# Kernel optimization log

Measured on AMD Instinct MI355X. Metric: run time of the kernel, lower is better.

Reference implementation:

```python
import jax, jax.numpy as jnp
import numpy as np


def setup_inputs() -> dict:
    key = jax.random.key(0)
    ks = jax.random.split(key, 6)
    B, Q, K = 4, 512, 1024
    Dq, Dk, Dv, H = 512, 512, 512, 128
    return {
        "queries": jax.random.normal(ks[0], (B, Q, Dq), dtype=jnp.float32),
        "keys": jax.random.normal(ks[1], (B, K, Dk), dtype=jnp.float32),
        "values": jax.random.normal(ks[2], (B, K, Dv), dtype=jnp.float32),
        "W_q": jax.random.normal(ks[3], (Dq, H), dtype=jnp.float32) / np.sqrt(Dq),
        "W_k": jax.random.normal(ks[4], (Dk, H), dtype=jnp.float32) / np.sqrt(Dk),
        "w_v": jax.random.normal(ks[5], (H,), dtype=jnp.float32) / np.sqrt(H),
    }


def reference(queries, keys, values, W_q, W_k, w_v):
    # Additive (Bahdanau) attention.
    q = jnp.einsum("bqd,dh->bqh", queries, W_q)          # [B,Q,H]
    k = jnp.einsum("bkd,dh->bkh", keys, W_k)             # [B,K,H]
    features = jnp.tanh(q[:, :, None, :] + k[:, None, :, :])  # [B,Q,K,H]
    scores = jnp.einsum("bqkh,h->bqk", features, w_v)    # [B,Q,K]
    attn = jax.nn.softmax(scores, axis=-1)               # [B,Q,K]
    return jnp.einsum("bqk,bkv->bqv", attn, values)      # [B,Q,Dv]
```

## Files before the change

### kernel.cpp

```cpp
#include <hip/hip_runtime.h>

#define BB   4
#define QS   512
#define KSZ  1024
#define DD   512
#define HH   128
#define DVV  512

typedef unsigned int uint;
typedef unsigned short ushort;
typedef __attribute__((ext_vector_type(8)))  short short8;
typedef __attribute__((ext_vector_type(16))) float f32x16;

__device__ __forceinline__ float rcp_fast(float x)  { return __builtin_amdgcn_rcpf(x); }
__device__ __forceinline__ float exp2_fast(float x) { return __builtin_amdgcn_exp2f(x); }

__device__ __forceinline__ void split1(float v, short& h, short& l) {
    uint u = __float_as_uint(v);
    h = (short)(u >> 16);
    float r = v - __uint_as_float(u & 0xffff0000u);
    l = (short)(__float_as_uint(r) >> 16);
}

__global__ __launch_bounds__(256) void proj_exp_kernel(
    const float* __restrict__ q,  const float* __restrict__ k,
    const float* __restrict__ Wq, const float* __restrict__ Wk,
    float* __restrict__ eq, float* __restrict__ ek, int nq_blocks)
{
    __shared__ float At[16][36];
    __shared__ float Wt[32][128];

    const float* A; const float* W; float* outp; int m0;
    if ((int)blockIdx.x < nq_blocks) {
        A = q;  W = Wq; outp = eq; m0 = blockIdx.x * 16;
    } else {
        A = k;  W = Wk; outp = ek; m0 = (blockIdx.x - nq_blocks) * 16;
    }

    const int tid = threadIdx.x;
    const int h4  = tid & 31;
    const int r   = tid >> 5;

    float4 acc0 = {0.f,0.f,0.f,0.f};
    float4 acc1 = {0.f,0.f,0.f,0.f};

    for (int d0 = 0; d0 < DD; d0 += 32) {
        if (tid < 128) {
            int row = tid >> 3, c4 = tid & 7;
            *(float4*)&At[row][c4 * 4] =
                *(const float4*)&A[(size_t)(m0 + row) * DD + d0 + c4 * 4];
        }
        #pragma unroll
        for (int i = 0; i < 4; i++) {
            int f = tid + i * 256;
            int row = f >> 5, c4 = f & 31;
            *(float4*)&Wt[row][c4 * 4] =
                *(const float4*)&W[(size_t)(d0 + row) * HH + c4 * 4];
        }
        __syncthreads();
        #pragma unroll 4
        for (int kk = 0; kk < 32; kk++) {
            float4 w4 = *(const float4*)&Wt[kk][h4 * 4];
            float a0 = At[r][kk];
            float a1 = At[r + 8][kk];
            acc0.x = fmaf(a0, w4.x, acc0.x); acc0.y = fmaf(a0, w4.y, acc0.y);
            acc0.z = fmaf(a0, w4.z, acc0.z); acc0.w = fmaf(a0, w4.w, acc0.w);
            acc1.x = fmaf(a1, w4.x, acc1.x); acc1.y = fmaf(a1, w4.y, acc1.y);
            acc1.z = fmaf(a1, w4.z, acc1.z); acc1.w = fmaf(a1, w4.w, acc1.w);
        }
        __syncthreads();
    }

    const float C2L = 2.8853900817779268f;
    float4 o0, o1;
    o0.x = exp2_fast(acc0.x * C2L); o0.y = exp2_fast(acc0.y * C2L);
    o0.z = exp2_fast(acc0.z * C2L); o0.w = exp2_fast(acc0.w * C2L);
    o1.x = exp2_fast(acc1.x * C2L); o1.y = exp2_fast(acc1.y * C2L);
    o1.z = exp2_fast(acc1.z * C2L); o1.w = exp2_fast(acc1.w * C2L);
    *(float4*)&outp[(size_t)(m0 + r)     * HH + h4 * 4] = o0;
    *(float4*)&outp[(size_t)(m0 + r + 8) * HH + h4 * 4] = o1;
}

__global__ __launch_bounds__(256) void vt_kernel(
    const float* __restrict__ val, ushort* __restrict__ vhi, ushort* __restrict__ vlo)
{
    __shared__ float Ts[32][33];
    const int b  = blockIdx.z;
    const int k0 = blockIdx.x * 32;
    const int n0 = blockIdx.y * 32;
    const int tid = threadIdx.x;

    {
        const int kk = tid >> 3, n4 = (tid & 7) * 4;
        float4 v = *(const float4*)&val[((size_t)b * KSZ + k0 + kk) * DVV + n0 + n4];
        Ts[kk][n4 + 0] = v.x; Ts[kk][n4 + 1] = v.y;
        Ts[kk][n4 + 2] = v.z; Ts[kk][n4 + 3] = v.w;
    }
    __syncthreads();
    {
        const int nn = tid >> 3, k4 = (tid & 7) * 4;
        ushort h[4], l[4];
        #pragma unroll
        for (int i = 0; i < 4; i++) {
            short hh, ll;
            split1(Ts[k4 + i][nn], hh, ll);
            h[i] = (ushort)hh; l[i] = (ushort)ll;
        }
        size_t o = ((size_t)b * DVV + n0 + nn) * KSZ + k0 + k4;
        *(ushort4*)&vhi[o] = make_ushort4(h[0], h[1], h[2], h[3]);
        *(ushort4*)&vlo[o] = make_ushort4(l[0], l[1], l[2], l[3]);
    }
}

__global__ __launch_bounds__(256) void scores_kernel(
    const float* __restrict__ eq, const float* __restrict__ ek,
    const float* __restrict__ wv, float* __restrict__ P, float* __restrict__ rsp)
{
    __shared__ float eqs[64][68];
    __shared__ float eks[64][68];
    __shared__ float wvs[HH];

    const int tid = threadIdx.x;
    const int b  = blockIdx.z;
    const int q0 = blockIdx.y * 64;
    const int k0 = blockIdx.x * 64;

    const float* eqb = eq + ((size_t)b * QS  + q0) * HH;
    const float* ekb = ek + ((size_t)b * KSZ + k0) * HH;

    if (tid < 32) *(float4*)&wvs[tid * 4] = *(const float4*)&wv[tid * 4];

    const int tk = tid & 15;
    const int tq = tid >> 4;

    float acc[4][4] = {};

    for (int hc = 0; hc < HH; hc += 64) {
        __syncthreads();
        #pragma unroll
        for (int i = 0; i < 4; i++) {
            int f = tid + i * 256;
            int row = f >> 4, c4 = f & 15;
            *(float4*)&eqs[row][c4 * 4] =
                *(const float4*)&eqb[(size_t)row * HH + hc + c4 * 4];
            *(float4*)&eks[row][c4 * 4] =
                *(const float4*)&ekb[(size_t)row * HH + hc + c4 * 4];
        }
        __syncthreads();

        for (int h0 = 0; h0 < 64; h0 += 4) {
            float4 wv4 = *(const float4*)&wvs[hc + h0];
            float4 eq4[4], ek4[4];
            #pragma unroll
            for (int j = 0; j < 4; j++) {
                eq4[j] = *(const float4*)&eqs[tq + 16 * j][h0];
                ek4[j] = *(const float4*)&eks[tk + 16 * j][h0];
            }
            #pragma unroll
            for (int jq = 0; jq < 4; jq++) {
                #pragma unroll
                for (int jk = 0; jk < 4; jk++) {
                    acc[jq][jk] = fmaf(wv4.x, rcp_fast(fmaf(eq4[jq].x, ek4[jk].x, 1.0f)), acc[jq][jk]);
                    acc[jq][jk] = fmaf(wv4.y, rcp_fast(fmaf(eq4[jq].y, ek4[jk].y, 1.0f)), acc[jq][jk]);
                    acc[jq][jk] = fmaf(wv4.z, rcp_fast(fmaf(eq4[jq].z, ek4[jk].z, 1.0f)), acc[jq][jk]);
                    acc[jq][jk] = fmaf(wv4.w, rcp_fast(fmaf(eq4[jq].w, ek4[jk].w, 1.0f)), acc[jq][jk]);
                }
            }
        }
    }

    const float CN = -2.8853900817779268f;
    float* pb = P + ((size_t)b * QS + q0) * KSZ + k0;
    #pragma unroll
    for (int jq = 0; jq < 4; jq++) {
        float rowp = 0.f;
        #pragma unroll
        for (int jk = 0; jk < 4; jk++) {
            float pv_ = exp2_fast(acc[jq][jk] * CN);
            pb[(size_t)(tq + 16 * jq) * KSZ + tk + 16 * jk] = pv_;
            rowp += pv_;
        }
        #pragma unroll
        for (int m = 8; m; m >>= 1) rowp += __shfl_xor(rowp, m);
        if ((tid & 15) == 0)
            rsp[((size_t)b * QS + q0 + tq + 16 * jq) * 16 + blockIdx.x] = rowp;
    }
}

__global__ __launch_bounds__(256) void pv_mfma_kernel(
    const float* __restrict__ P, const ushort* __restrict__ vhi,
    const ushort* __restrict__ vlo, const float* __restrict__ rsp,
    float* __restrict__ outp)
{
    __shared__ float invs[64];

    const int id = blockIdx.x;
    const int x  = id & 7;
    const int j  = id >> 3;
    const int bm = x * 4 + (j >> 3);
    const int nt = j & 7;
    const int b  = bm >> 3, mt = bm & 7;

    const int tid = threadIdx.x, w = tid >> 6, lane = tid & 63;

    if (tid < 64) {
        const float* rp = rsp + ((size_t)b * QS + mt * 64 + tid) * 16;
        float s = 0.f;
        #pragma unroll
        for (int i = 0; i < 16; i++) s += rp[i];
        invs[tid] = rcp_fast(s);
    }
    __syncthreads();

    const int mw = mt * 64 + (w & 1) * 32;
    const int nw = nt * 64 + (w >> 1) * 32;
    const int row = lane & 31, kg = lane >> 5;

    const float*  pa = P   + ((size_t)b * QS  + mw + row) * KSZ;
    const ushort* bh = vhi + ((size_t)b * DVV + nw + row) * KSZ;
    const ushort* bl = vlo + ((size_t)b * DVV + nw + row) * KSZ;

    f32x16 acc;
    #pragma unroll
    for (int i = 0; i < 16; i++) acc[i] = 0.f;

    #pragma unroll 4
    for (int kb = 0; kb < KSZ; kb += 16) {
        const int ka = kb + kg * 8;
        float4 p0 = *(const float4*)(pa + ka);
        float4 p1 = *(const float4*)(pa + ka + 4);
        short8 vh = *(const short8*)(bh + ka);
        short8 vl = *(const short8*)(bl + ka);
        short8 ah, al;
        {
            float v[8] = {p0.x, p0.y, p0.z, p0.w, p1.x, p1.y, p1.z, p1.w};
            #pragma unroll
            for (int i = 0; i < 8; i++) {
                short hh, ll; split1(v[i], hh, ll);
                ah[i] = hh; al[i] = ll;
            }
        }
        acc = __builtin_amdgcn_mfma_f32_32x32x16_bf16(ah, vh, acc, 0, 0, 0);
        acc = __builtin_amdgcn_mfma_f32_32x32x16_bf16(ah, vl, acc, 0, 0, 0);
        acc = __builtin_amdgcn_mfma_f32_32x32x16_bf16(al, vh, acc, 0, 0, 0);
    }

    float* ob = outp + ((size_t)b * QS + mt * 64) * DVV + nt * 64 + (w >> 1) * 32;
    const int col = lane & 31;
    #pragma unroll
    for (int r = 0; r < 16; r++) {
        const int rb = (w & 1) * 32 + (r & 3) + 8 * (r >> 2) + 4 * kg;
        ob[(size_t)rb * DVV + col] = acc[r] * invs[rb];
    }
}

extern "C" void kernel_launch(void* const* d_in, const int* in_sizes, int n_in,
                              void* d_out, int out_size, void* d_ws, size_t ws_size,
                              hipStream_t stream)
{
    const float* queries = (const float*)d_in[0];
    const float* keys    = (const float*)d_in[1];
    const float* values  = (const float*)d_in[2];
    const float* Wq      = (const float*)d_in[3];
    const float* Wk      = (const float*)d_in[4];
    const float* wv      = (const float*)d_in[5];
    float* out = (float*)d_out;

    float* eq  = (float*)d_ws;
    float* ek  = eq  + (size_t)BB * QS * HH;
    float* P   = ek  + (size_t)BB * KSZ * HH;
    float* rsp = P   + (size_t)BB * QS * KSZ;
    ushort* vhi = (ushort*)(rsp + (size_t)BB * QS * 16);
    ushort* vlo = vhi + (size_t)BB * KSZ * DVV;

    vt_kernel<<<dim3(KSZ / 32, DVV / 32, BB), 256, 0, stream>>>(values, vhi, vlo);

    const int nq_blocks = BB * QS / 16;
    const int nk_blocks = BB * KSZ / 16;
    proj_exp_kernel<<<dim3(nq_blocks + nk_blocks), 256, 0, stream>>>(
        queries, keys, Wq, Wk, eq, ek, nq_blocks);

    scores_kernel<<<dim3(KSZ / 64, QS / 64, BB), 256, 0, stream>>>(eq, ek, wv, P, rsp);

    pv_mfma_kernel<<<dim3(256), 256, 0, stream>>>(P, vhi, vlo, rsp, out);
}
```

Baseline: 165.8 us.

## Fuse value transpose into projection kernel, pre-split P to bf16, split-K PV

Merges the value transpose/bf16 split and the query/key projection into a single prep launch, and halves the rows per projection block so more blocks run. The scores kernel now writes P as separate bf16 hi/lo arrays, so the PV kernel loads ready MFMA operands instead of splitting floats in its inner loop. The PV kernel splits K across warp pairs with an LDS reduction and uses 512 blocks for more parallelism. The cost is more scattered 2-byte stores in the scores kernel, an extra LDS reduction step, and a scalar global read of wv in place of its shared-memory copy.

```diff
diff --git a/kernel.cpp b/kernel.cpp
--- a/kernel.cpp
+++ b/kernel.cpp
@@ -15,37 +15,67 @@
 __device__ __forceinline__ float rcp_fast(float x)  { return __builtin_amdgcn_rcpf(x); }
 __device__ __forceinline__ float exp2_fast(float x) { return __builtin_amdgcn_exp2f(x); }
 
-__device__ __forceinline__ void split1(float v, short& h, short& l) {
+__device__ __forceinline__ void split1(float v, ushort& h, ushort& l) {
     uint u = __float_as_uint(v);
-    h = (short)(u >> 16);
+    h = (ushort)(u >> 16);
     float r = v - __uint_as_float(u & 0xffff0000u);
-    l = (short)(__float_as_uint(r) >> 16);
-}
-
-__global__ __launch_bounds__(256) void proj_exp_kernel(
+    l = (ushort)(__float_as_uint(r) >> 16);
+}
+
+#define NVT (BB * (KSZ / 32) * (DVV / 32))
+#define NQ8 (BB * QS / 8)
+#define NK8 (BB * KSZ / 8)
+
+__global__ __launch_bounds__(256) void prep_kernel(
     const float* __restrict__ q,  const float* __restrict__ k,
+    const float* __restrict__ val,
     const float* __restrict__ Wq, const float* __restrict__ Wk,
-    float* __restrict__ eq, float* __restrict__ ek, int nq_blocks)
-{
-    __shared__ float At[16][36];
+    float* __restrict__ eq, float* __restrict__ ek,
+    ushort* __restrict__ vhi, ushort* __restrict__ vlo)
+{
+    const int id  = blockIdx.x;
+    const int tid = threadIdx.x;
+
+    if (id < NVT) {
+        __shared__ float Ts[32][33];
+        const int b   = id >> 9;
+        const int rem = id & 511;
+        const int k0  = (rem >> 4) * 32;
+        const int n0  = (rem & 15) * 32;
+        {
+            const int kk = tid >> 3, n4 = (tid & 7) * 4;
+            float4 v = *(const float4*)&val[((size_t)b * KSZ + k0 + kk) * DVV + n0 + n4];
+            Ts[kk][n4 + 0] = v.x; Ts[kk][n4 + 1] = v.y;
+            Ts[kk][n4 + 2] = v.z; Ts[kk][n4 + 3] = v.w;
+        }
+        __syncthreads();
+        {
+            const int nn = tid >> 3, k4 = (tid & 7) * 4;
+            ushort h[4], l[4];
+            #pragma unroll
+            for (int i = 0; i < 4; i++) split1(Ts[k4 + i][nn], h[i], l[i]);
+            size_t o = ((size_t)b * DVV + n0 + nn) * KSZ + k0 + k4;
+            *(ushort4*)&vhi[o] = make_ushort4(h[0], h[1], h[2], h[3]);
+            *(ushort4*)&vlo[o] = make_ushort4(l[0], l[1], l[2], l[3]);
+        }
+        return;
+    }
+
+    __shared__ float At[8][36];
     __shared__ float Wt[32][128];
 
+    const int pid = id - NVT;
     const float* A; const float* W; float* outp; int m0;
-    if ((int)blockIdx.x < nq_blocks) {
-        A = q;  W = Wq; outp = eq; m0 = blockIdx.x * 16;
-    } else {
-        A = k;  W = Wk; outp = ek; m0 = (blockIdx.x - nq_blocks) * 16;
-    }
-
-    const int tid = threadIdx.x;
-    const int h4  = tid & 31;
-    const int r   = tid >> 5;
-
-    float4 acc0 = {0.f,0.f,0.f,0.f};
-    float4 acc1 = {0.f,0.f,0.f,0.f};
+    if (pid < NQ8) { A = q; W = Wq; outp = eq; m0 = pid * 8; }
+    else           { A = k; W = Wk; outp = ek; m0 = (pid - NQ8) * 8; }
+
+    const int h4 = tid & 31;
+    const int r  = tid >> 5;
+
+    float4 acc = {0.f, 0.f, 0.f, 0.f};
 
     for (int d0 = 0; d0 < DD; d0 += 32) {
-        if (tid < 128) {
+        if (tid < 64) {
             int row = tid >> 3, c4 = tid & 7;
             *(float4*)&At[row][c4 * 4] =
                 *(const float4*)&A[(size_t)(m0 + row) * DD + d0 + c4 * 4];
@@ -58,67 +88,30 @@
                 *(const float4*)&W[(size_t)(d0 + row) * HH + c4 * 4];
         }
         __syncthreads();
-        #pragma unroll 4
+        #pragma unroll 8
         for (int kk = 0; kk < 32; kk++) {
             float4 w4 = *(const float4*)&Wt[kk][h4 * 4];
             float a0 = At[r][kk];
-            float a1 = At[r + 8][kk];
-            acc0.x = fmaf(a0, w4.x, acc0.x); acc0.y = fmaf(a0, w4.y, acc0.y);
-            acc0.z = fmaf(a0, w4.z, acc0.z); acc0.w = fmaf(a0, w4.w, acc0.w);
-            acc1.x = fmaf(a1, w4.x, acc1.x); acc1.y = fmaf(a1, w4.y, acc1.y);
-            acc1.z = fmaf(a1, w4.z, acc1.z); acc1.w = fmaf(a1, w4.w, acc1.w);
+            acc.x = fmaf(a0, w4.x, acc.x); acc.y = fmaf(a0, w4.y, acc.y);
+            acc.z = fmaf(a0, w4.z, acc.z); acc.w = fmaf(a0, w4.w, acc.w);
         }
         __syncthreads();
     }
 
     const float C2L = 2.8853900817779268f;
-    float4 o0, o1;
-    o0.x = exp2_fast(acc0.x * C2L); o0.y = exp2_fast(acc0.y * C2L);
-    o0.z = exp2_fast(acc0.z * C2L); o0.w = exp2_fast(acc0.w * C2L);
-    o1.x = exp2_fast(acc1.x * C2L); o1.y = exp2_fast(acc1.y * C2L);
-    o1.z = exp2_fast(acc1.z * C2L); o1.w = exp2_fast(acc1.w * C2L);
-    *(float4*)&outp[(size_t)(m0 + r)     * HH + h4 * 4] = o0;
-    *(float4*)&outp[(size_t)(m0 + r + 8) * HH + h4 * 4] = o1;
-}
-
-__global__ __launch_bounds__(256) void vt_kernel(
-    const float* __restrict__ val, ushort* __restrict__ vhi, ushort* __restrict__ vlo)
-{
-    __shared__ float Ts[32][33];
-    const int b  = blockIdx.z;
-    const int k0 = blockIdx.x * 32;
-    const int n0 = blockIdx.y * 32;
-    const int tid = threadIdx.x;
-
-    {
-        const int kk = tid >> 3, n4 = (tid & 7) * 4;
-        float4 v = *(const float4*)&val[((size_t)b * KSZ + k0 + kk) * DVV + n0 + n4];
-        Ts[kk][n4 + 0] = v.x; Ts[kk][n4 + 1] = v.y;
-        Ts[kk][n4 + 2] = v.z; Ts[kk][n4 + 3] = v.w;
-    }
-    __syncthreads();
-    {
-        const int nn = tid >> 3, k4 = (tid & 7) * 4;
-        ushort h[4], l[4];
-        #pragma unroll
-        for (int i = 0; i < 4; i++) {
-            short hh, ll;
-            split1(Ts[k4 + i][nn], hh, ll);
-            h[i] = (ushort)hh; l[i] = (ushort)ll;
-        }
-        size_t o = ((size_t)b * DVV + n0 + nn) * KSZ + k0 + k4;
-        *(ushort4*)&vhi[o] = make_ushort4(h[0], h[1], h[2], h[3]);
-        *(ushort4*)&vlo[o] = make_ushort4(l[0], l[1], l[2], l[3]);
-    }
+    float4 o;
+    o.x = exp2_fast(acc.x * C2L); o.y = exp2_fast(acc.y * C2L);
+    o.z = exp2_fast(acc.z * C2L); o.w = exp2_fast(acc.w * C2L);
+    *(float4*)&outp[(size_t)(m0 + r) * HH + h4 * 4] = o;
 }
 
 __global__ __launch_bounds__(256) void scores_kernel(
     const float* __restrict__ eq, const float* __restrict__ ek,
-    const float* __restrict__ wv, float* __restrict__ P, float* __restrict__ rsp)
+    const float* __restrict__ wv, ushort* __restrict__ Phi,
+    ushort* __restrict__ Plo, float* __restrict__ rsp)
 {
     __shared__ float eqs[64][68];
     __shared__ float eks[64][68];
-    __shared__ float wvs[HH];
 
     const int tid = threadIdx.x;
     const int b  = blockIdx.z;
@@ -127,8 +120,6 @@
 
     const float* eqb = eq + ((size_t)b * QS  + q0) * HH;
     const float* ekb = ek + ((size_t)b * KSZ + k0) * HH;
-
-    if (tid < 32) *(float4*)&wvs[tid * 4] = *(const float4*)&wv[tid * 4];
 
     const int tk = tid & 15;
     const int tq = tid >> 4;
@@ -149,7 +140,7 @@
         __syncthreads();
 
         for (int h0 = 0; h0 < 64; h0 += 4) {
-            float4 wv4 = *(const float4*)&wvs[hc + h0];
+            float4 wv4 = *(const float4*)&wv[hc + h0];
             float4 eq4[4], ek4[4];
             #pragma unroll
             for (int j = 0; j < 4; j++) {
@@ -170,14 +161,17 @@
     }
 
     const float CN = -2.8853900817779268f;
-    float* pb = P + ((size_t)b * QS + q0) * KSZ + k0;
+    ushort* ph = Phi + ((size_t)b * QS + q0) * KSZ + k0;
+    ushort* pl = Plo + ((size_t)b * QS + q0) * KSZ + k0;
     #pragma unroll
     for (int jq = 0; jq < 4; jq++) {
         float rowp = 0.f;
         #pragma unroll
         for (int jk = 0; jk < 4; jk++) {
             float pv_ = exp2_fast(acc[jq][jk] * CN);
-            pb[(size_t)(tq + 16 * jq) * KSZ + tk + 16 * jk] = pv_;
+            ushort hh, ll; split1(pv_, hh, ll);
+            size_t o = (size_t)(tq + 16 * jq) * KSZ + tk + 16 * jk;
+            ph[o] = hh; pl[o] = ll;
             rowp += pv_;
         }
         #pragma unroll
@@ -188,18 +182,19 @@
 }
 
 __global__ __launch_bounds__(256) void pv_mfma_kernel(
-    const float* __restrict__ P, const ushort* __restrict__ vhi,
-    const ushort* __restrict__ vlo, const float* __restrict__ rsp,
-    float* __restrict__ outp)
+    const ushort* __restrict__ Phi, const ushort* __restrict__ Plo,
+    const ushort* __restrict__ vhi, const ushort* __restrict__ vlo,
+    const float* __restrict__ rsp, float* __restrict__ outp)
 {
     __shared__ float invs[64];
+    __shared__ float accs[2][32][33];
 
     const int id = blockIdx.x;
     const int x  = id & 7;
     const int j  = id >> 3;
-    const int bm = x * 4 + (j >> 3);
-    const int nt = j & 7;
-    const int b  = bm >> 3, mt = bm & 7;
+    const int b  = x >> 1;
+    const int mt = (x & 1) * 4 + (j >> 4);
+    const int nt = j & 15;
 
     const int tid = threadIdx.x, w = tid >> 6, lane = tid & 63;
 
@@ -210,47 +205,47 @@
         for (int i = 0; i < 16; i++) s += rp[i];
         invs[tid] = rcp_fast(s);
     }
-    __syncthreads();
-
-    const int mw = mt * 64 + (w & 1) * 32;
-    const int nw = nt * 64 + (w >> 1) * 32;
+
+    const int mw  = mt * 64 + (w & 1) * 32;
+    const int kh  = (w >> 1) * (KSZ / 2);
     const int row = lane & 31, kg = lane >> 5;
-
-    const float*  pa = P   + ((size_t)b * QS  + mw + row) * KSZ;
-    const ushort* bh = vhi + ((size_t)b * DVV + nw + row) * KSZ;
-    const ushort* bl = vlo + ((size_t)b * DVV + nw + row) * KSZ;
+    const int nb  = nt * 32;
+
+    const ushort* pah = Phi + ((size_t)b * QS  + mw + row) * KSZ + kh;
+    const ushort* pal = Plo + ((size_t)b * QS  + mw + row) * KSZ + kh;
+    const ushort* bhp = vhi + ((size_t)b * DVV + nb + row) * KSZ + kh;
+    const ushort* blp = vlo + ((size_t)b * DVV + nb + row) * KSZ + kh;
 
     f32x16 acc;
     #pragma unroll
     for (int i = 0; i < 16; i++) acc[i] = 0.f;
 
-    #pragma unroll 4
-    for (int kb = 0; kb < KSZ; kb += 16) {
+    #pragma unroll 8
+    for (int kb = 0; kb < KSZ / 2; kb += 16) {
         const int ka = kb + kg * 8;
-        float4 p0 = *(const float4*)(pa + ka);
-        float4 p1 = *(const float4*)(pa + ka + 4);
-        short8 vh = *(const short8*)(bh + ka);
-        short8 vl = *(const short8*)(bl + ka);
-        short8 ah, al;
-        {
-            float v[8] = {p0.x, p0.y, p0.z, p0.w, p1.x, p1.y, p1.z, p1.w};
-            #pragma unroll
-            for (int i = 0; i < 8; i++) {
-                short hh, ll; split1(v[i], hh, ll);
-                ah[i] = hh; al[i] = ll;
-            }
-        }
+        short8 ah = *(const short8*)(pah + ka);
+        short8 al = *(const short8*)(pal + ka);
+        short8 vh = *(const short8*)(bhp + ka);
+        short8 vl = *(const short8*)(blp + ka);
         acc = __builtin_amdgcn_mfma_f32_32x32x16_bf16(ah, vh, acc, 0, 0, 0);
         acc = __builtin_amdgcn_mfma_f32_32x32x16_bf16(ah, vl, acc, 0, 0, 0);
         acc = __builtin_amdgcn_mfma_f32_32x32x16_bf16(al, vh, acc, 0, 0, 0);
     }
 
-    float* ob = outp + ((size_t)b * QS + mt * 64) * DVV + nt * 64 + (w >> 1) * 32;
-    const int col = lane & 31;
-    #pragma unroll
-    for (int r = 0; r < 16; r++) {
-        const int rb = (w & 1) * 32 + (r & 3) + 8 * (r >> 2) + 4 * kg;
-        ob[(size_t)rb * DVV + col] = acc[r] * invs[rb];
+    if (w >= 2) {
+        #pragma unroll
+        for (int r = 0; r < 16; r++)
+            accs[w - 2][(r & 3) + 8 * (r >> 2) + 4 * kg][row] = acc[r];
+    }
+    __syncthreads();
+    if (w < 2) {
+        float* ob = outp + ((size_t)b * QS + mw) * DVV + nb;
+        #pragma unroll
+        for (int r = 0; r < 16; r++) {
+            const int rb = (r & 3) + 8 * (r >> 2) + 4 * kg;
+            float v = acc[r] + accs[w][rb][row];
+            ob[(size_t)rb * DVV + row] = v * invs[(w & 1) * 32 + rb];
+        }
     }
 }
 
@@ -266,21 +261,19 @@
     const float* wv      = (const float*)d_in[5];
     float* out = (float*)d_out;
 
-    float* eq  = (float*)d_ws;
-    float* ek  = eq  + (size_t)BB * QS * HH;
-    float* P   = ek  + (size_t)BB * KSZ * HH;
-    float* rsp = P   + (size_t)BB * QS * KSZ;
-    ushort* vhi = (ushort*)(rsp + (size_t)BB * QS * 16);
+    float*  eq  = (float*)d_ws;
+    float*  ek  = eq + (size_t)BB * QS * HH;
+    float*  rsp = ek + (size_t)BB * KSZ * HH;
+    ushort* Phi = (ushort*)(rsp + (size_t)BB * QS * 16);
+    ushort* Plo = Phi + (size_t)BB * QS * KSZ;
+    ushort* vhi = Plo + (size_t)BB * QS * KSZ;
     ushort* vlo = vhi + (size_t)BB * KSZ * DVV;
 
-    vt_kernel<<<dim3(KSZ / 32, DVV / 32, BB), 256, 0, stream>>>(values, vhi, vlo);
-
-    const int nq_blocks = BB * QS / 16;
-    const int nk_blocks = BB * KSZ / 16;
-    proj_exp_kernel<<<dim3(nq_blocks + nk_blocks), 256, 0, stream>>>(
-        queries, keys, Wq, Wk, eq, ek, nq_blocks);
-
-    scores_kernel<<<dim3(KSZ / 64, QS / 64, BB), 256, 0, stream>>>(eq, ek, wv, P, rsp);
-
-    pv_mfma_kernel<<<dim3(256), 256, 0, stream>>>(P, vhi, vlo, rsp, out);
-}
+    prep_kernel<<<dim3(NVT + NQ8 + NK8), 256, 0, stream>>>(
+        queries, keys, values, Wq, Wk, eq, ek, vhi, vlo);
+
+    scores_kernel<<<dim3(KSZ / 64, QS / 64, BB), 256, 0, stream>>>(
+        eq, ek, wv, Phi, Plo, rsp);
+
+    pv_mfma_kernel<<<dim3(512), 256, 0, stream>>>(Phi, Plo, vhi, vlo, rsp, out);
+}
```

Result: slower. 170.1 us (+2.6%).
